# Performance work log

Measured on AMD Instinct MI355X. Metric: run time of the kernel, lower is better.

The kernel has to match this reference:

```python
import jax, jax.numpy as jnp
import numpy as np

DIM = 1024
HEADS = 16
HEAD_DIM = DIM // HEADS
EPS = 1e-5


def setup_inputs() -> dict:
    key = jax.random.key(0)
    ks = jax.random.split(key, 4)
    N, L = 4, 2048
    x = jax.random.normal(ks[0], (N, L, DIM), dtype=jnp.float32)
    # causal mask: True means masked (strictly upper triangle)
    attn_mask = jnp.triu(jnp.ones((L, L), dtype=jnp.bool_), k=1)[None, None, :, :]
    w_qkv = jax.random.normal(ks[1], (3 * DIM, DIM), dtype=jnp.float32) * (DIM ** -0.5)
    w_proj = jax.random.normal(ks[2], (DIM, DIM), dtype=jnp.float32) * (DIM ** -0.5)
    b_proj = jnp.zeros((DIM,), dtype=jnp.float32)
    q_gamma = jnp.ones((HEAD_DIM,), dtype=jnp.float32)
    q_beta = jnp.zeros((HEAD_DIM,), dtype=jnp.float32)
    k_gamma = jnp.ones((HEAD_DIM,), dtype=jnp.float32)
    k_beta = jnp.zeros((HEAD_DIM,), dtype=jnp.float32)
    return {"x": x, "attn_mask": attn_mask, "w_qkv": w_qkv, "w_proj": w_proj,
            "b_proj": b_proj, "q_gamma": q_gamma, "q_beta": q_beta,
            "k_gamma": k_gamma, "k_beta": k_beta}


def _layernorm(h, gamma, beta):
    mu = jnp.mean(h, axis=-1, keepdims=True)
    var = jnp.mean(jnp.square(h - mu), axis=-1, keepdims=True)
    return (h - mu) * jax.lax.rsqrt(var + EPS) * gamma + beta


def reference(x, attn_mask, w_qkv, w_proj, b_proj, q_gamma, q_beta, k_gamma, k_beta):
    N, L, D = x.shape
    H, hd = HEADS, HEAD_DIM
    scale = hd ** -0.5
    qkv = jnp.einsum('nld,ed->nle', x, w_qkv)  # [N, L, 3D]
    qkv = qkv.reshape(N, L, 3, H, hd).transpose(2, 0, 3, 1, 4)  # [3, N, H, L, hd]
    q, k, v = qkv[0], qkv[1], qkv[2]
    q = _layernorm(q, q_gamma, q_beta)
    k = _layernorm(k, k_gamma, k_beta)
    scores = jnp.einsum('nhqd,nhkd->nhqk', q * scale, k)
    scores = scores + jnp.where(attn_mask, -jnp.inf, 0.0).astype(scores.dtype)
    attn = jax.nn.softmax(scores, axis=-1)
    out = jnp.einsum('nhqk,nhkd->nhqd', attn, v)  # [N, H, L, hd]
    out = out.transpose(0, 2, 1, 3).reshape(N, L, D)
    return jnp.einsum('nld,ed->nle', out, w_proj) + b_proj
```

## Files before the change

kernel.cpp:

```cpp
#include <hip/hip_runtime.h>


using f16x8 = __attribute__((ext_vector_type(8))) _Float16;
using f16x4 = __attribute__((ext_vector_type(4))) _Float16;
using f16x2 = __attribute__((ext_vector_type(2))) _Float16;
using f32x4 = __attribute__((ext_vector_type(4))) float;
using f32x16 = __attribute__((ext_vector_type(16))) float;
using u32x4 = __attribute__((ext_vector_type(4))) unsigned int;

#define MFMA16(a, b, c) __builtin_amdgcn_mfma_f32_16x16x32_f16(a, b, c, 0, 0, 0)
#define MFMA32(a, b, c) __builtin_amdgcn_mfma_f32_32x32x16_f16(a, b, c, 0, 0, 0)

__device__ __forceinline__ void gload_lds16(const void* g, void* l) {
  __builtin_amdgcn_global_load_lds(
      (const __attribute__((address_space(1))) unsigned int*)g,
      (__attribute__((address_space(3))) unsigned int*)l, 16, 0, 0);
}

__device__ __forceinline__ float dot2acc(unsigned int pk, float c) {
#if __has_builtin(__builtin_amdgcn_fdot2)
  const f16x2 ones = {(_Float16)1.f, (_Float16)1.f};
  return __builtin_amdgcn_fdot2(__builtin_bit_cast(f16x2, pk), ones, c, false);
#else
  f16x2 v = __builtin_bit_cast(f16x2, pk);
  return c + (float)v[0] + (float)v[1];
#endif
}

__global__ __launch_bounds__(256) void f32_to_f16_kernel(
    const float* __restrict__ in, _Float16* __restrict__ out, int n) {
  int i = (blockIdx.x * 256 + threadIdx.x) * 8;
  if (i >= n) return;
  float4 a = *(const float4*)(in + i);
  float4 b = *(const float4*)(in + i + 4);
  f16x8 o;
  o[0] = (_Float16)a.x; o[1] = (_Float16)a.y; o[2] = (_Float16)a.z; o[3] = (_Float16)a.w;
  o[4] = (_Float16)b.x; o[5] = (_Float16)b.y; o[6] = (_Float16)b.z; o[7] = (_Float16)b.w;
  *(f16x8*)(out + i) = o;
}

template <int MODE>
__global__ __launch_bounds__(256) void gemm_bt(
    const _Float16* __restrict__ A, const _Float16* __restrict__ B,
    void* __restrict__ Cout, const float* __restrict__ bias,
    const float* __restrict__ qg, const float* __restrict__ qb,
    const float* __restrict__ kg, const float* __restrict__ kb,
    int M, int N, int K) {
  __shared__ __align__(16) _Float16 As[128 * 32];
  __shared__ __align__(16) _Float16 Bs[128 * 32];
  const int tid = threadIdx.x;
  const int w = tid >> 6, lane = tid & 63;
  const int c = lane & 15, g = lane >> 4;
  const long mbase = (long)blockIdx.x * 128;
  const long nbase = (long)blockIdx.y * 128;
  const int wm = (w >> 1) * 64, wn = (w & 1) * 64;
  const int srow = w * 32 + (lane >> 2);
  const int scol = ((lane & 3) ^ ((lane >> 3) & 3)) * 8;
  const int sg = (g ^ ((c >> 1) & 3)) * 8;

  f32x4 acc[4][4];
#pragma unroll
  for (int i = 0; i < 4; ++i)
#pragma unroll
    for (int j = 0; j < 4; ++j) acc[i][j] = f32x4{0.f, 0.f, 0.f, 0.f};

  for (int kt = 0; kt < K; kt += 32) {
    __syncthreads();
    gload_lds16(A + (mbase + srow) * K + kt + scol, As + w * 1024);
    gload_lds16(A + (mbase + srow + 16) * K + kt + scol, As + w * 1024 + 512);
    gload_lds16(B + (nbase + srow) * K + kt + scol, Bs + w * 1024);
    gload_lds16(B + (nbase + srow + 16) * K + kt + scol, Bs + w * 1024 + 512);
    __syncthreads();
    f16x8 af[4], bfr[4];
#pragma unroll
    for (int mt = 0; mt < 4; ++mt)
      af[mt] = *(const f16x8*)(As + (wm + mt * 16 + c) * 32 + sg);
#pragma unroll
    for (int nt = 0; nt < 4; ++nt)
      bfr[nt] = *(const f16x8*)(Bs + (wn + nt * 16 + c) * 32 + sg);
#pragma unroll
    for (int mt = 0; mt < 4; ++mt)
#pragma unroll
      for (int nt = 0; nt < 4; ++nt)
        acc[mt][nt] = MFMA16(af[mt], bfr[nt], acc[mt][nt]);
  }

  if constexpr (MODE == 1) {
    const int region = (int)(nbase >> 10);
    if (region < 2) {
      const float* gamma = region ? kg : qg;
      const float* beta = region ? kb : qb;
      float gam[4], bet[4];
#pragma unroll
      for (int nt = 0; nt < 4; ++nt) {
        gam[nt] = gamma[nt * 16 + c];
        bet[nt] = beta[nt * 16 + c];
      }
      const float sc = region ? 1.f : 0.1803368801111204f;
#pragma unroll
      for (int mt = 0; mt < 4; ++mt)
#pragma unroll
        for (int r = 0; r < 4; ++r) {
          float s1 = 0.f, s2 = 0.f;
#pragma unroll
          for (int nt = 0; nt < 4; ++nt) {
            const float v = acc[mt][nt][r];
            s1 += v;
            s2 += v * v;
          }
#pragma unroll
          for (int msk = 1; msk < 16; msk <<= 1) {
            s1 += __shfl_xor(s1, msk);
            s2 += __shfl_xor(s2, msk);
          }
          const float mu = s1 * 0.015625f;
          const float rstd = rsqrtf(s2 * 0.015625f - mu * mu + 1e-5f);
#pragma unroll
          for (int nt = 0; nt < 4; ++nt)
            acc[mt][nt][r] =
                ((acc[mt][nt][r] - mu) * rstd * gam[nt] + bet[nt]) * sc;
        }
    }
#pragma unroll
    for (int nt = 0; nt < 4; ++nt) {
      const long col = nbase + wn + nt * 16 + c;
#pragma unroll
      for (int mt = 0; mt < 4; ++mt)
#pragma unroll
        for (int r = 0; r < 4; ++r) {
          const long row = mbase + wm + mt * 16 + g * 4 + r;
          ((_Float16*)Cout)[row * N + col] = (_Float16)acc[mt][nt][r];
        }
    }
  } else {
#pragma unroll
    for (int nt = 0; nt < 4; ++nt) {
      const long col = nbase + wn + nt * 16 + c;
      const float bv = bias ? bias[col] : 0.f;
#pragma unroll
      for (int mt = 0; mt < 4; ++mt)
#pragma unroll
        for (int r = 0; r < 4; ++r) {
          const long row = mbase + wm + mt * 16 + g * 4 + r;
          ((float*)Cout)[row * N + col] = acc[mt][nt][r] + bv;
        }
    }
  }
}

__global__ __launch_bounds__(256) void transpose_v_kernel(
    const _Float16* __restrict__ qkv, _Float16* __restrict__ Vt) {
  __shared__ __align__(16) _Float16 tile[64][80];
  const int nh = blockIdx.y;
  const long n = nh >> 4;
  const int h = nh & 15;
  const long lbase = (long)blockIdx.x * 64;
  const int t = threadIdx.x;
#pragma unroll
  for (int r = 0; r < 2; ++r) {
    const int l = (t + r * 256) >> 3;
    const int cc = (t & 7) * 8;
    f16x8 v = *(const f16x8*)(qkv + (n * 2048 + lbase + l) * 3072 + 2048 + h * 64 + cc);
    *(f16x8*)&tile[l][cc] = v;
  }
  __syncthreads();
  const int d = t >> 2, q = t & 3;
  f16x8 o0, o1;
#pragma unroll
  for (int i = 0; i < 8; ++i) {
    o0[i] = tile[q * 16 + i][d];
    o1[i] = tile[q * 16 + 8 + i][d];
  }
  _Float16* dst = Vt + ((long)nh * 64 + d) * 2048 + lbase + q * 16;
  *(f16x8*)dst = o0;
  *(f16x8*)(dst + 8) = o1;
}

__global__ __launch_bounds__(256) void attn_kernel(
    const _Float16* __restrict__ qkv, const _Float16* __restrict__ Vt,
    _Float16* __restrict__ Ob) {
  __shared__ __align__(16) _Float16 Ks[2][64 * 64];
  __shared__ __align__(16) _Float16 Vs[2][64 * 64];
  const int w = threadIdx.x >> 6;
  const int lane = threadIdx.x & 63;
  const int c5 = lane & 31;
  const int hi = lane >> 5;
  const int nh = blockIdx.x;
  const long n = nh >> 4;
  const int h = nh & 15;
  const int qtile = 15 - blockIdx.y;
  const int qlo_blk = qtile * 128;
  const int qlo = qlo_blk + w * 32;
  const int qrow = qlo + c5;

  const _Float16* Qp = qkv + n * 2048 * 3072 + h * 64;
  const _Float16* Kq = Qp + 1024;
  const _Float16* Vp = Vt + (long)nh * 64 * 2048;

  const int sr8 = lane >> 3;
  const int scol = ((lane & 7) ^ sr8) * 8;

  const int nkv_blk = (qlo_blk + 191) >> 6;
  const int nkv_w = (qlo + 95) >> 6;

  const float NEG_M = -12.0f;

#define STAGE(buf, kv)                                                        \
  {                                                                           \
    const int kb_ = (kv) * 64;                                                \
    _Pragma("unroll") for (int i = 0; i < 2; ++i) {                           \
      const int idx = w * 2 + i;                                              \
      const int row = idx * 8 + sr8;                                          \
      gload_lds16(Kq + (long)(kb_ + row) * 3072 + scol, &Ks[buf][idx * 512]); \
      gload_lds16(Vp + (long)row * 2048 + kb_ + scol, &Vs[buf][idx * 512]);   \
    }                                                                         \
  }

  f16x8 qf[4];
#pragma unroll
  for (int dc = 0; dc < 4; ++dc)
    qf[dc] = *(const f16x8*)(Qp + (long)qrow * 3072 + dc * 16 + hi * 8);

  f32x16 acc[2];
#pragma unroll
  for (int db = 0; db < 2; ++db)
#pragma unroll
    for (int r = 0; r < 16; ++r) acc[db][r] = 0.f;
  float ls = 0.f;

  STAGE(0, 0);

  const int swr = c5 & 7;

  for (int kv = 0; kv < nkv_blk; ++kv) {
    const int cur = kv & 1;
    __syncthreads();
    if (kv + 1 < nkv_blk) STAGE(cur ^ 1, kv + 1);

    if (kv < nkv_w) {
      const int kbase = kv * 64;
      const _Float16* Kb = Ks[cur];
      const _Float16* Vb = Vs[cur];
      f32x16 s0, s1;
#pragma unroll
      for (int r = 0; r < 16; ++r) { s0[r] = NEG_M; s1[r] = NEG_M; }
      __builtin_amdgcn_s_setprio(1);
#pragma unroll
      for (int dc = 0; dc < 4; ++dc) {
        const int b = (dc * 2 + hi) ^ swr;
        f16x8 kf0 = *(const f16x8*)(Kb + c5 * 64 + b * 8);
        f16x8 kf1 = *(const f16x8*)(Kb + (32 + c5) * 64 + b * 8);
        s0 = MFMA32(kf0, qf[dc], s0);
        s1 = MFMA32(kf1, qf[dc], s1);
      }
      __builtin_amdgcn_s_setprio(0);
      if (kbase + 63 > qlo) {
#pragma unroll
        for (int r = 0; r < 16; ++r) {
          const int mv = (r & 3) + 8 * (r >> 2) + 4 * hi;
          if (kbase + mv > qrow) s0[r] = -1e30f;
          if (kbase + 32 + mv > qrow) s1[r] = -1e30f;
        }
      }
#pragma unroll
      for (int r = 0; r < 16; ++r) {
        s0[r] = exp2f(s0[r]);
        s1[r] = exp2f(s1[r]);
      }
      unsigned int pk0[4][2], pk1[4][2];
#pragma unroll
      for (int r2 = 0; r2 < 4; ++r2)
#pragma unroll
        for (int p = 0; p < 2; ++p) {
          pk0[r2][p] = __builtin_bit_cast(
              unsigned int,
              __builtin_amdgcn_cvt_pkrtz(s0[4 * r2 + 2 * p], s0[4 * r2 + 2 * p + 1]));
          pk1[r2][p] = __builtin_bit_cast(
              unsigned int,
              __builtin_amdgcn_cvt_pkrtz(s1[4 * r2 + 2 * p], s1[4 * r2 + 2 * p + 1]));
        }
#pragma unroll
      for (int r2 = 0; r2 < 4; ++r2)
#pragma unroll
        for (int p = 0; p < 2; ++p) {
          ls = dot2acc(pk0[r2][p], ls);
          ls = dot2acc(pk1[r2][p], ls);
        }
      f16x8 pB[4];
#pragma unroll
      for (int kk = 0; kk < 4; ++kk) {
        const int rx = (kk & 1) * 2;
        unsigned int x0 = (kk < 2) ? pk0[rx][0] : pk1[rx][0];
        unsigned int y0 = (kk < 2) ? pk0[rx + 1][0] : pk1[rx + 1][0];
        unsigned int x1 = (kk < 2) ? pk0[rx][1] : pk1[rx][1];
        unsigned int y1 = (kk < 2) ? pk0[rx + 1][1] : pk1[rx + 1][1];
        asm("v_permlane32_swap_b32 %0, %1" : "+v"(x0), "+v"(y0));
        asm("v_permlane32_swap_b32 %0, %1" : "+v"(x1), "+v"(y1));
        pB[kk] = __builtin_bit_cast(f16x8, u32x4{x0, x1, y0, y1});
      }
      __builtin_amdgcn_s_setprio(1);
#pragma unroll
      for (int db = 0; db < 2; ++db)
#pragma unroll
        for (int kk = 0; kk < 4; ++kk) {
          const int rowd = db * 32 + c5;
          const int bb = (kk * 2 + hi) ^ swr;
          f16x8 vf = *(const f16x8*)(Vb + rowd * 64 + bb * 8);
          acc[db] = MFMA32(vf, pB[kk], acc[db]);
        }
      __builtin_amdgcn_s_setprio(0);
    }
  }
  const float lsr = ls + __shfl_xor(ls, 32);
  const float inv = 1.f / lsr;
  _Float16* ob = Ob + ((long)(n * 2048) + qrow) * 1024 + h * 64 + 4 * hi;
#pragma unroll
  for (int db = 0; db < 2; ++db)
#pragma unroll
    for (int r2 = 0; r2 < 4; ++r2) {
      f16x4 o;
#pragma unroll
      for (int j = 0; j < 4; ++j)
        o[j] = (_Float16)(acc[db][4 * r2 + j] * inv);
      *(f16x4*)(ob + db * 32 + 8 * r2) = o;
    }
#undef STAGE
}

extern "C" void kernel_launch(void* const* d_in, const int* in_sizes, int n_in,
                              void* d_out, int out_size, void* d_ws, size_t ws_size,
                              hipStream_t stream) {
  const float* x = (const float*)d_in[0];
  const float* w_qkv = (const float*)d_in[2];
  const float* w_proj = (const float*)d_in[3];
  const float* b_proj = (const float*)d_in[4];
  const float* qg = (const float*)d_in[5];
  const float* qb = (const float*)d_in[6];
  const float* kg = (const float*)d_in[7];
  const float* kb = (const float*)d_in[8];

  char* ws = (char*)d_ws;
  _Float16* xb     = (_Float16*)(ws + 0);
  _Float16* wqkvb  = (_Float16*)(ws + 16777216);
  _Float16* wprojb = (_Float16*)(ws + 23068672);
  _Float16* qkvh   = (_Float16*)(ws + 25165824);
  _Float16* Vt     = (_Float16*)(ws + 75497472);
  _Float16* Ob     = xb;

  f32_to_f16_kernel<<<4096, 256, 0, stream>>>(x, xb, 8388608);
  f32_to_f16_kernel<<<1536, 256, 0, stream>>>(w_qkv, wqkvb, 3145728);
  f32_to_f16_kernel<<<512, 256, 0, stream>>>(w_proj, wprojb, 1048576);

  gemm_bt<1><<<dim3(64, 24), 256, 0, stream>>>(xb, wqkvb, qkvh, nullptr,
                                               qg, qb, kg, kb, 8192, 3072, 1024);
  transpose_v_kernel<<<dim3(32, 64), 256, 0, stream>>>(qkvh, Vt);
  attn_kernel<<<dim3(64, 16), 256, 0, stream>>>(qkvh, Vt, Ob);
  gemm_bt<0><<<dim3(64, 8), 256, 0, stream>>>(Ob, wprojb, d_out, b_proj,
                                              nullptr, nullptr, nullptr, nullptr,
                                              8192, 1024, 1024);
}
```

Baseline: 214.9 us.

## Double-buffer GEMM LDS tiles and feed constant accumulator into first attention MFMA

The GEMM main loop now uses two LDS buffers per operand and prefetches the next K-slice while computing the current one, which drops one barrier per iteration. MFMA priority is also raised around the GEMM inner product. In the attention kernel, the per-iteration initialization of the score accumulators to the -12 offset is replaced by passing a hoisted constant vector as the C operand of the first MFMA. This doubles GEMM LDS usage, which may reduce occupancy.

```diff
diff --git a/kernel.cpp b/kernel.cpp
--- a/kernel.cpp
+++ b/kernel.cpp
@@ -46,8 +46,8 @@
     const float* __restrict__ qg, const float* __restrict__ qb,
     const float* __restrict__ kg, const float* __restrict__ kb,
     int M, int N, int K) {
-  __shared__ __align__(16) _Float16 As[128 * 32];
-  __shared__ __align__(16) _Float16 Bs[128 * 32];
+  __shared__ __align__(16) _Float16 As[2][128 * 32];
+  __shared__ __align__(16) _Float16 Bs[2][128 * 32];
   const int tid = threadIdx.x;
   const int w = tid >> 6, lane = tid & 63;
   const int c = lane & 15, g = lane >> 4;
@@ -58,32 +58,45 @@
   const int scol = ((lane & 3) ^ ((lane >> 3) & 3)) * 8;
   const int sg = (g ^ ((c >> 1) & 3)) * 8;
 
+#define GSTAGE(buf, kt_)                                                      \
+  {                                                                           \
+    const int kk_ = (kt_) * 32;                                               \
+    gload_lds16(A + (mbase + srow) * K + kk_ + scol, &As[buf][w * 1024]);     \
+    gload_lds16(A + (mbase + srow + 16) * K + kk_ + scol,                     \
+                &As[buf][w * 1024 + 512]);                                    \
+    gload_lds16(B + (nbase + srow) * K + kk_ + scol, &Bs[buf][w * 1024]);     \
+    gload_lds16(B + (nbase + srow + 16) * K + kk_ + scol,                     \
+                &Bs[buf][w * 1024 + 512]);                                    \
+  }
+
   f32x4 acc[4][4];
 #pragma unroll
   for (int i = 0; i < 4; ++i)
 #pragma unroll
     for (int j = 0; j < 4; ++j) acc[i][j] = f32x4{0.f, 0.f, 0.f, 0.f};
 
-  for (int kt = 0; kt < K; kt += 32) {
+  const int nk = K >> 5;
+  GSTAGE(0, 0);
+  for (int kt = 0; kt < nk; ++kt) {
+    const int cur = kt & 1;
     __syncthreads();
-    gload_lds16(A + (mbase + srow) * K + kt + scol, As + w * 1024);
-    gload_lds16(A + (mbase + srow + 16) * K + kt + scol, As + w * 1024 + 512);
-    gload_lds16(B + (nbase + srow) * K + kt + scol, Bs + w * 1024);
-    gload_lds16(B + (nbase + srow + 16) * K + kt + scol, Bs + w * 1024 + 512);
-    __syncthreads();
+    if (kt + 1 < nk) GSTAGE(cur ^ 1, kt + 1);
     f16x8 af[4], bfr[4];
 #pragma unroll
     for (int mt = 0; mt < 4; ++mt)
-      af[mt] = *(const f16x8*)(As + (wm + mt * 16 + c) * 32 + sg);
+      af[mt] = *(const f16x8*)(&As[cur][(wm + mt * 16 + c) * 32 + sg]);
 #pragma unroll
     for (int nt = 0; nt < 4; ++nt)
-      bfr[nt] = *(const f16x8*)(Bs + (wn + nt * 16 + c) * 32 + sg);
+      bfr[nt] = *(const f16x8*)(&Bs[cur][(wn + nt * 16 + c) * 32 + sg]);
+    __builtin_amdgcn_s_setprio(1);
 #pragma unroll
     for (int mt = 0; mt < 4; ++mt)
 #pragma unroll
       for (int nt = 0; nt < 4; ++nt)
         acc[mt][nt] = MFMA16(af[mt], bfr[nt], acc[mt][nt]);
-  }
+    __builtin_amdgcn_s_setprio(0);
+  }
+#undef GSTAGE
 
   if constexpr (MODE == 1) {
     const int region = (int)(nbase >> 10);
@@ -203,8 +216,6 @@
   const int nkv_blk = (qlo_blk + 191) >> 6;
   const int nkv_w = (qlo + 95) >> 6;
 
-  const float NEG_M = -12.0f;
-
 #define STAGE(buf, kv)                                                        \
   {                                                                           \
     const int kb_ = (kv) * 64;                                                \
@@ -221,6 +232,10 @@
   for (int dc = 0; dc < 4; ++dc)
     qf[dc] = *(const f16x8*)(Qp + (long)qrow * 3072 + dc * 16 + hi * 8);
 
+  f32x16 negM;
+#pragma unroll
+  for (int r = 0; r < 16; ++r) negM[r] = -12.0f;
+
   f32x16 acc[2];
 #pragma unroll
   for (int db = 0; db < 2; ++db)
@@ -242,11 +257,16 @@
       const _Float16* Kb = Ks[cur];
       const _Float16* Vb = Vs[cur];
       f32x16 s0, s1;
-#pragma unroll
-      for (int r = 0; r < 16; ++r) { s0[r] = NEG_M; s1[r] = NEG_M; }
       __builtin_amdgcn_s_setprio(1);
-#pragma unroll
-      for (int dc = 0; dc < 4; ++dc) {
+      {
+        const int b = hi ^ swr;
+        f16x8 kf0 = *(const f16x8*)(Kb + c5 * 64 + b * 8);
+        f16x8 kf1 = *(const f16x8*)(Kb + (32 + c5) * 64 + b * 8);
+        s0 = MFMA32(kf0, qf[0], negM);
+        s1 = MFMA32(kf1, qf[0], negM);
+      }
+#pragma unroll
+      for (int dc = 1; dc < 4; ++dc) {
         const int b = (dc * 2 + hi) ^ swr;
         f16x8 kf0 = *(const f16x8*)(Kb + c5 * 64 + b * 8);
         f16x8 kf1 = *(const f16x8*)(Kb + (32 + c5) * 64 + b * 8);
```

New measurement: 210.3 us. 2.1% less time.
